# Optimization experiments

Measured on AMD Instinct MI355X. Metric: run time of the kernel, lower is better.

Reference implementation:

```python
import jax, jax.numpy as jnp
import numpy as np

B, S, H = 8, 2048, 2048

def setup_inputs() -> dict:
    key = jax.random.key(0)
    ks = jax.random.split(key, 7)
    return {
        "time_decay": jax.random.normal(ks[0], (H,), dtype=jnp.float32),
        "key": jax.random.normal(ks[1], (B, S, H), dtype=jnp.float32),
        "time_first": jax.random.normal(ks[2], (H,), dtype=jnp.float32),
        "value": jax.random.normal(ks[3], (B, S, H), dtype=jnp.float32),
        "max_state": jax.random.normal(ks[4], (B, H), dtype=jnp.float32),
        "num_state": jax.random.normal(ks[5], (B, H), dtype=jnp.float32),
        "den_state": jax.random.uniform(ks[6], (B, H), dtype=jnp.float32),
    }

def _wkv(time_decay, k, time_first, v, max_state, num_state, den_state):
    f32 = jnp.float32
    td = -jnp.exp(time_decay.astype(f32))          # [H]
    tf = time_first.astype(f32)                    # [H]
    k = k.astype(f32)
    v = v.astype(f32)

    def step(carry, kv_t):
        m, num, den = carry                        # each [B,H]
        kt, vt = kv_t                              # each [B,H]
        # output branch: include time_first bonus
        mo = jnp.maximum(m, kt + tf)
        e1o = jnp.exp(m - mo)
        e2o = jnp.exp(kt + tf - mo)
        out = (e1o * num + e2o * vt) / (e1o * den + e2o)
        # state branch: apply decay
        ms = jnp.maximum(m + td, kt)
        e1s = jnp.exp(m + td - ms)
        e2s = jnp.exp(kt - ms)
        return (ms, e1s * num + e2s * vt, e1s * den + e2s), out

    carry0 = (max_state.astype(f32), num_state.astype(f32), den_state.astype(f32))
    # scan over time: move seq axis to front -> [S,B,H]
    (m, num, den), outs = jax.lax.scan(
        step, carry0, (jnp.swapaxes(k, 0, 1), jnp.swapaxes(v, 0, 1)))
    output = jnp.swapaxes(outs, 0, 1)              # [B,S,H]
    return output, m, num, den

def reference(time_decay, key, time_first, value, max_state, num_state, den_state):
    return _wkv(time_decay, key, time_first, value, max_state, num_state, den_state)
```

## Files before the change

kernel.cpp:

```cpp
#include <hip/hip_runtime.h>


#define TILE 128
#define NW   16
#define SUB  (TILE / NW)

#define BARR  asm volatile("s_waitcnt lgkmcnt(0)\n\ts_barrier" ::: "memory")

__device__ __forceinline__ float ex2(float x)  { return __builtin_amdgcn_exp2f(x); }
__device__ __forceinline__ float rcpf(float x) { return __builtin_amdgcn_rcpf(x); }

__global__ __launch_bounds__(1024)
void wkv_fwd(const float* __restrict__ td_in, const float* __restrict__ kin,
             const float* __restrict__ tf_in, const float* __restrict__ vin,
             const float* __restrict__ m0, const float* __restrict__ n0,
             const float* __restrict__ d0,
             float* __restrict__ out, float* __restrict__ m_out,
             float* __restrict__ n_out, float* __restrict__ dn_out,
             int B, int S, int H)
{
    __shared__ float smry[2][NW][3][64];
    __shared__ float cry[2][3][64];

    const int tid  = threadIdx.x;
    const int lane = tid & 63;
    const int w    = tid >> 6;

    const int bpb = H >> 6;
    const int b   = blockIdx.x / bpb;
    const int hb  = (blockIdx.x - b * bpb) << 6;
    const int h   = hb + lane;
    const int g   = b * H + h;

    constexpr float Cc = 1.4426950408889634f;
    constexpr float IC = 0.6931471805599453f;

    const float tds  = -ex2(td_in[h] * Cc) * Cc;
    const float tfs  = tf_in[h] * Cc;
    const float dseg = tds * (float)SUB;

    if (w == 0) {
        cry[0][0][lane] = m0[g] * Cc;
        cry[0][1][lane] = n0[g];
        cry[0][2][lane] = d0[g];
    }

    const size_t base = (size_t)b * (size_t)S * (size_t)H + (size_t)hb;
    const float* gk = kin + base;
    const float* gv = vin + base;
    float*       go = out + base;

    const int ntiles = S / TILE;

    float fM = 0.f, fN = 0.f, fD = 0.f;

    float ka[SUB], va[SUB], kb[SUB], vb[SUB];

    {
        const size_t t0 = (size_t)w * SUB;
        #pragma unroll
        for (int j = 0; j < SUB; ++j) {
            ka[j] = gk[(t0 + j) * (size_t)H + lane];
            va[j] = gv[(t0 + j) * (size_t)H + lane];
        }
    }

    auto body = [&](int it, float (&ck)[SUB], float (&cv)[SUB],
                    float (&nk)[SUB], float (&nv)[SUB])
                __attribute__((always_inline)) -> void {
        if (it + 1 < ntiles) {
            const size_t t1 = (size_t)(it + 1) * TILE + (size_t)w * SUB;
            #pragma unroll
            for (int j = 0; j < SUB; ++j) {
                nk[j] = gk[(t1 + j) * (size_t)H + lane];
                nv[j] = gv[(t1 + j) * (size_t)H + lane];
            }
        }

        const int p = it & 1;

        float kt[SUB], vt[SUB];
        float plm[SUB - 1], pln[SUB - 1], pld[SUB - 1];
        float lm = -1e30f, ln = 0.f, ld = 0.f;
        #pragma unroll
        for (int j = 0; j < SUB; ++j) {
            kt[j] = ck[j] * Cc;
            vt[j] = cv[j];
            const float mpd = lm + tds;
            const float d   = mpd - kt[j];
            const float e   = ex2(-fabsf(d));
            const bool  c   = d >= 0.f;
            const float e1  = c ? 1.f : e;
            const float e2  = c ? e : 1.f;
            ln  = e1 * ln  + e2 * vt[j];
            ld  = e1 * ld  + e2;
            lm  = fmaxf(mpd, kt[j]);
            if (j < SUB - 1) { plm[j] = lm; pln[j] = ln; pld[j] = ld; }
        }
        smry[p][w][0][lane] = lm;
        smry[p][w][1][lane] = ln;
        smry[p][w][2][lane] = ld;
        BARR;

        float M = cry[p][0][lane];
        float N = cry[p][1][lane];
        float D = cry[p][2][lane];
        #pragma unroll
        for (int j = 0; j < NW - 1; ++j) {
            const float sm = smry[p][j][0][lane];
            const float sn = smry[p][j][1][lane];
            const float sd = smry[p][j][2][lane];
            if (j < w) {
                const float Md = M + dseg;
                const float d  = Md - sm;
                const float e  = ex2(-fabsf(d));
                const bool  c  = d >= 0.f;
                const float a  = c ? 1.f : e;
                const float bb = c ? e : 1.f;
                N = a * N + bb * sn;
                D = a * D + bb * sd;
                M = fmaxf(Md, sm);
            }
        }

        if (w == NW - 1) {
            const float Md = M + dseg;
            const float d  = Md - lm;
            const float e  = ex2(-fabsf(d));
            const bool  c  = d >= 0.f;
            const float a  = c ? 1.f : e;
            const float bb = c ? e : 1.f;
            fN = a * N + bb * ln;
            fD = a * D + bb * ld;
            fM = fmaxf(Md, lm);
            cry[p ^ 1][0][lane] = fM;
            cry[p ^ 1][1][lane] = fN;
            cry[p ^ 1][2][lane] = fD;
        }

        float* po = go + ((size_t)it * TILE + (size_t)w * SUB) * (size_t)H;
        {
            const float ktf = kt[0] + tfs;
            const float dd  = M - ktf;
            const float eo  = ex2(-fabsf(dd));
            const bool  co  = dd >= 0.f;
            const float e1o = co ? 1.f : eo;
            const float e2o = co ? eo : 1.f;
            po[lane] = (e1o * N + e2o * vt[0]) * rcpf(fmaf(e1o, D, e2o));
        }
        float Md = M;
        #pragma unroll
        for (int j = 1; j < SUB; ++j) {
            Md += tds;
            const float sm = plm[j - 1];
            const float dl = Md - sm;
            const float e  = ex2(-fabsf(dl));
            const bool  c  = dl >= 0.f;
            const float a  = c ? 1.f : e;
            const float bb = c ? e : 1.f;
            const float Nc = a * N + bb * pln[j - 1];
            const float Dc = a * D + bb * pld[j - 1];
            const float Mc = fmaxf(Md, sm);
            const float ktf = kt[j] + tfs;
            const float dd  = Mc - ktf;
            const float eo  = ex2(-fabsf(dd));
            const bool  co  = dd >= 0.f;
            const float e1o = co ? 1.f : eo;
            const float e2o = co ? eo : 1.f;
            po[(size_t)j * H + lane] =
                (e1o * Nc + e2o * vt[j]) * rcpf(fmaf(e1o, Dc, e2o));
        }
    };

    int it = 0;
    for (; it + 1 < ntiles; it += 2) {
        body(it,     ka, va, kb, vb);
        body(it + 1, kb, vb, ka, va);
    }
    if (it < ntiles) body(it, ka, va, kb, vb);

    if (w == NW - 1) {
        m_out[g]  = fM * IC;
        n_out[g]  = fN;
        dn_out[g] = fD;
    }
}

__global__ __launch_bounds__(64)
void wkv_fwd_serial(const float* __restrict__ td_in, const float* __restrict__ kin,
                    const float* __restrict__ tf_in, const float* __restrict__ vin,
                    const float* __restrict__ m0, const float* __restrict__ n0,
                    const float* __restrict__ d0,
                    float* __restrict__ out, float* __restrict__ m_out,
                    float* __restrict__ n_out, float* __restrict__ dn_out,
                    int B, int S, int H)
{
    const int g = blockIdx.x * 64 + threadIdx.x;
    if (g >= B * H) return;
    const int b = g / H;
    const int h = g - b * H;
    constexpr float Cc = 1.4426950408889634f, IC = 0.6931471805599453f;
    const float tds = -ex2(td_in[h] * Cc) * Cc;
    const float tfs = tf_in[h] * Cc;
    float M = m0[g] * Cc, N = n0[g], D = d0[g];
    const size_t base = (size_t)b * S * H + h;
    for (int t = 0; t < S; ++t) {
        const float kt  = kin[base + (size_t)t * H] * Cc;
        const float vt  = vin[base + (size_t)t * H];
        const float ktf = kt + tfs;
        const float mo  = fmaxf(M, ktf);
        const float e1o = ex2(M - mo), e2o = ex2(ktf - mo);
        out[base + (size_t)t * H] = (e1o * N + e2o * vt) * rcpf(e1o * D + e2o);
        const float mpd = M + tds;
        const float ms  = fmaxf(mpd, kt);
        const float e1s = ex2(mpd - ms), e2s = ex2(kt - ms);
        N = e1s * N + e2s * vt;
        D = e1s * D + e2s;
        M = ms;
    }
    m_out[g] = M * IC; n_out[g] = N; dn_out[g] = D;
}

extern "C" void kernel_launch(void* const* d_in, const int* in_sizes, int n_in,
                              void* d_out, int out_size, void* d_ws, size_t ws_size,
                              hipStream_t stream)
{
    const float* time_decay = (const float*)d_in[0];
    const float* key        = (const float*)d_in[1];
    const float* time_first = (const float*)d_in[2];
    const float* value      = (const float*)d_in[3];
    const float* max_state  = (const float*)d_in[4];
    const float* num_state  = (const float*)d_in[5];
    const float* den_state  = (const float*)d_in[6];

    const int H  = in_sizes[0];
    const int BH = in_sizes[4];
    const int B  = BH / H;
    const int S  = in_sizes[1] / BH;

    float* out    = (float*)d_out;
    float* m_out  = out + (size_t)B * (size_t)S * (size_t)H;
    float* n_out  = m_out + BH;
    float* dn_out = n_out + BH;

    if ((H % 64 == 0) && (S % TILE == 0)) {
        const int grid = BH / 64;
        wkv_fwd<<<grid, 1024, 0, stream>>>(time_decay, key, time_first, value,
                                           max_state, num_state, den_state,
                                           out, m_out, n_out, dn_out, B, S, H);
    } else {
        const int grid = (BH + 63) / 64;
        wkv_fwd_serial<<<grid, 64, 0, stream>>>(time_decay, key, time_first, value,
                                                max_state, num_state, den_state,
                                                out, m_out, n_out, dn_out, B, S, H);
    }
}
```

Before: 337.0 us.

## Split each wave across two time segments per 32-channel group with shuffle merge

Each block now covers 32 channels instead of 64. The two half-waves each scan a separate 8-step segment of a 256-step tile, and their summaries are merged with a cross-lane shuffle before the block-level scan. The per-step prefix states are no longer stored. Outputs are instead produced by re-running the recurrence from the merged segment prefix. The grid doubles, which raises parallelism and occupancy, at the cost of half-wave 32-float global accesses and an extra merge step.

Result: slower. 496.4 us (+47.3%).

```diff
diff --git a/kernel.cpp b/kernel.cpp
--- a/kernel.cpp
+++ b/kernel.cpp
@@ -1,16 +1,31 @@
 #include <hip/hip_runtime.h>
 
 
-#define TILE 128
-#define NW   16
-#define SUB  (TILE / NW)
+#define TILE   256
+#define NW     16
+#define WSTEPS 16
+#define SUBL   8
 
 #define BARR  asm volatile("s_waitcnt lgkmcnt(0)\n\ts_barrier" ::: "memory")
 
 __device__ __forceinline__ float ex2(float x)  { return __builtin_amdgcn_exp2f(x); }
 __device__ __forceinline__ float rcpf(float x) { return __builtin_amdgcn_rcpf(x); }
 
-__global__ __launch_bounds__(1024)
+__device__ __forceinline__ void merge(float& M, float& N, float& D,
+                                      float dlen, float sm, float sn, float sd)
+{
+    const float Md = M + dlen;
+    const float d  = Md - sm;
+    const float e  = ex2(-fabsf(d));
+    const bool  c  = d >= 0.f;
+    const float a  = c ? 1.f : e;
+    const float bb = c ? e : 1.f;
+    N = a * N + bb * sn;
+    D = a * D + bb * sd;
+    M = fmaxf(Md, sm);
+}
+
+__global__ __launch_bounds__(1024, 8)
 void wkv_fwd(const float* __restrict__ td_in, const float* __restrict__ kin,
              const float* __restrict__ tf_in, const float* __restrict__ vin,
              const float* __restrict__ m0, const float* __restrict__ n0,
@@ -19,30 +34,33 @@
              float* __restrict__ n_out, float* __restrict__ dn_out,
              int B, int S, int H)
 {
-    __shared__ float smry[2][NW][3][64];
-    __shared__ float cry[2][3][64];
+    __shared__ float smry[2][NW][3][32];
+    __shared__ float cry[2][3][32];
 
     const int tid  = threadIdx.x;
     const int lane = tid & 63;
     const int w    = tid >> 6;
-
-    const int bpb = H >> 6;
+    const int c    = lane & 31;
+    const int s    = lane >> 5;
+
+    const int bpb = H >> 5;
     const int b   = blockIdx.x / bpb;
-    const int hb  = (blockIdx.x - b * bpb) << 6;
-    const int h   = hb + lane;
+    const int hb  = (blockIdx.x - b * bpb) << 5;
+    const int h   = hb + c;
     const int g   = b * H + h;
 
     constexpr float Cc = 1.4426950408889634f;
     constexpr float IC = 0.6931471805599453f;
 
-    const float tds  = -ex2(td_in[h] * Cc) * Cc;
-    const float tfs  = tf_in[h] * Cc;
-    const float dseg = tds * (float)SUB;
-
-    if (w == 0) {
-        cry[0][0][lane] = m0[g] * Cc;
-        cry[0][1][lane] = n0[g];
-        cry[0][2][lane] = d0[g];
+    const float tds    = -ex2(td_in[h] * Cc) * Cc;
+    const float tfs    = tf_in[h] * Cc;
+    const float dseg8  = tds * (float)SUBL;
+    const float dseg16 = tds * (float)WSTEPS;
+
+    if (w == 0 && s == 0) {
+        cry[0][0][c] = m0[g] * Cc;
+        cry[0][1][c] = n0[g];
+        cry[0][2][c] = d0[g];
     }
 
     const size_t base = (size_t)b * (size_t)S * (size_t)H + (size_t)hb;
@@ -50,125 +68,111 @@
     const float* gv = vin + base;
     float*       go = out + base;
 
+    const int row0   = w * WSTEPS + s * SUBL;
     const int ntiles = S / TILE;
 
     float fM = 0.f, fN = 0.f, fD = 0.f;
 
-    float ka[SUB], va[SUB], kb[SUB], vb[SUB];
-
-    {
-        const size_t t0 = (size_t)w * SUB;
-        #pragma unroll
-        for (int j = 0; j < SUB; ++j) {
-            ka[j] = gk[(t0 + j) * (size_t)H + lane];
-            va[j] = gv[(t0 + j) * (size_t)H + lane];
-        }
-    }
-
-    auto body = [&](int it, float (&ck)[SUB], float (&cv)[SUB],
-                    float (&nk)[SUB], float (&nv)[SUB])
+    float ka[SUBL], va[SUBL], kb[SUBL], vb[SUBL];
+
+    #pragma unroll
+    for (int j = 0; j < SUBL; ++j) {
+        ka[j] = gk[(size_t)(row0 + j) * (size_t)H + c];
+        va[j] = gv[(size_t)(row0 + j) * (size_t)H + c];
+    }
+
+    auto body = [&](int it, float (&ck)[SUBL], float (&cv)[SUBL],
+                    float (&nk)[SUBL], float (&nv)[SUBL])
                 __attribute__((always_inline)) -> void {
         if (it + 1 < ntiles) {
-            const size_t t1 = (size_t)(it + 1) * TILE + (size_t)w * SUB;
+            const size_t r1 = (size_t)(it + 1) * TILE + row0;
             #pragma unroll
-            for (int j = 0; j < SUB; ++j) {
-                nk[j] = gk[(t1 + j) * (size_t)H + lane];
-                nv[j] = gv[(t1 + j) * (size_t)H + lane];
+            for (int j = 0; j < SUBL; ++j) {
+                nk[j] = gk[(r1 + j) * (size_t)H + c];
+                nv[j] = gv[(r1 + j) * (size_t)H + c];
             }
         }
 
         const int p = it & 1;
 
-        float kt[SUB], vt[SUB];
-        float plm[SUB - 1], pln[SUB - 1], pld[SUB - 1];
         float lm = -1e30f, ln = 0.f, ld = 0.f;
         #pragma unroll
-        for (int j = 0; j < SUB; ++j) {
-            kt[j] = ck[j] * Cc;
-            vt[j] = cv[j];
+        for (int j = 0; j < SUBL; ++j) {
+            const float kt = ck[j] * Cc;
+            ck[j] = kt;
+            const float vt  = cv[j];
             const float mpd = lm + tds;
-            const float d   = mpd - kt[j];
+            const float d   = mpd - kt;
             const float e   = ex2(-fabsf(d));
-            const bool  c   = d >= 0.f;
-            const float e1  = c ? 1.f : e;
-            const float e2  = c ? e : 1.f;
-            ln  = e1 * ln  + e2 * vt[j];
-            ld  = e1 * ld  + e2;
-            lm  = fmaxf(mpd, kt[j]);
-            if (j < SUB - 1) { plm[j] = lm; pln[j] = ln; pld[j] = ld; }
-        }
-        smry[p][w][0][lane] = lm;
-        smry[p][w][1][lane] = ln;
-        smry[p][w][2][lane] = ld;
+            const bool  cc  = d >= 0.f;
+            const float e1  = cc ? 1.f : e;
+            const float e2  = cc ? e : 1.f;
+            ln = e1 * ln + e2 * vt;
+            ld = e1 * ld + e2;
+            lm = fmaxf(mpd, kt);
+        }
+
+        const float om = __shfl_xor(lm, 32);
+        const float on = __shfl_xor(ln, 32);
+        const float od = __shfl_xor(ld, 32);
+
+        float wm = s ? om : lm, wn = s ? on : ln, wd = s ? od : ld;
+        {
+            const float sm2 = s ? lm : om;
+            const float sn2 = s ? ln : on;
+            const float sd2 = s ? ld : od;
+            merge(wm, wn, wd, dseg8, sm2, sn2, sd2);
+        }
+        if (s == 0) {
+            smry[p][w][0][c] = wm;
+            smry[p][w][1][c] = wn;
+            smry[p][w][2][c] = wd;
+        }
         BARR;
 
-        float M = cry[p][0][lane];
-        float N = cry[p][1][lane];
-        float D = cry[p][2][lane];
+        float M = cry[p][0][c];
+        float N = cry[p][1][c];
+        float D = cry[p][2][c];
         #pragma unroll
         for (int j = 0; j < NW - 1; ++j) {
-            const float sm = smry[p][j][0][lane];
-            const float sn = smry[p][j][1][lane];
-            const float sd = smry[p][j][2][lane];
-            if (j < w) {
-                const float Md = M + dseg;
-                const float d  = Md - sm;
-                const float e  = ex2(-fabsf(d));
-                const bool  c  = d >= 0.f;
-                const float a  = c ? 1.f : e;
-                const float bb = c ? e : 1.f;
-                N = a * N + bb * sn;
-                D = a * D + bb * sd;
-                M = fmaxf(Md, sm);
-            }
-        }
-
-        if (w == NW - 1) {
-            const float Md = M + dseg;
-            const float d  = Md - lm;
-            const float e  = ex2(-fabsf(d));
-            const bool  c  = d >= 0.f;
-            const float a  = c ? 1.f : e;
-            const float bb = c ? e : 1.f;
-            fN = a * N + bb * ln;
-            fD = a * D + bb * ld;
-            fM = fmaxf(Md, lm);
-            cry[p ^ 1][0][lane] = fM;
-            cry[p ^ 1][1][lane] = fN;
-            cry[p ^ 1][2][lane] = fD;
-        }
-
-        float* po = go + ((size_t)it * TILE + (size_t)w * SUB) * (size_t)H;
-        {
-            const float ktf = kt[0] + tfs;
+            const float sm = smry[p][j][0][c];
+            const float sn = smry[p][j][1][c];
+            const float sd = smry[p][j][2][c];
+            if (j < w) merge(M, N, D, dseg16, sm, sn, sd);
+        }
+
+        if (w == NW - 1 && s == 0) {
+            fM = M; fN = N; fD = D;
+            merge(fM, fN, fD, dseg16, wm, wn, wd);
+            cry[p ^ 1][0][c] = fM;
+            cry[p ^ 1][1][c] = fN;
+            cry[p ^ 1][2][c] = fD;
+        }
+
+        if (s == 1) merge(M, N, D, dseg8, om, on, od);
+
+        float* po = go + ((size_t)it * TILE + row0) * (size_t)H;
+        #pragma unroll
+        for (int j = 0; j < SUBL; ++j) {
+            const float kt  = ck[j];
+            const float vt  = cv[j];
+            const float ktf = kt + tfs;
             const float dd  = M - ktf;
             const float eo  = ex2(-fabsf(dd));
             const bool  co  = dd >= 0.f;
             const float e1o = co ? 1.f : eo;
             const float e2o = co ? eo : 1.f;
-            po[lane] = (e1o * N + e2o * vt[0]) * rcpf(fmaf(e1o, D, e2o));
-        }
-        float Md = M;
-        #pragma unroll
-        for (int j = 1; j < SUB; ++j) {
-            Md += tds;
-            const float sm = plm[j - 1];
-            const float dl = Md - sm;
-            const float e  = ex2(-fabsf(dl));
-            const bool  c  = dl >= 0.f;
-            const float a  = c ? 1.f : e;
-            const float bb = c ? e : 1.f;
-            const float Nc = a * N + bb * pln[j - 1];
-            const float Dc = a * D + bb * pld[j - 1];
-            const float Mc = fmaxf(Md, sm);
-            const float ktf = kt[j] + tfs;
-            const float dd  = Mc - ktf;
-            const float eo  = ex2(-fabsf(dd));
-            const bool  co  = dd >= 0.f;
-            const float e1o = co ? 1.f : eo;
-            const float e2o = co ? eo : 1.f;
-            po[(size_t)j * H + lane] =
-                (e1o * Nc + e2o * vt[j]) * rcpf(fmaf(e1o, Dc, e2o));
+            po[(size_t)j * H + c] =
+                (e1o * N + e2o * vt) * rcpf(fmaf(e1o, D, e2o));
+            const float mpd = M + tds;
+            const float ds_ = mpd - kt;
+            const float es  = ex2(-fabsf(ds_));
+            const bool  cs  = ds_ >= 0.f;
+            const float e1s = cs ? 1.f : es;
+            const float e2s = cs ? es : 1.f;
+            N = e1s * N + e2s * vt;
+            D = e1s * D + e2s;
+            M = fmaxf(mpd, kt);
         }
     };
 
@@ -179,7 +183,7 @@
     }
     if (it < ntiles) body(it, ka, va, kb, vb);
 
-    if (w == NW - 1) {
+    if (w == NW - 1 && s == 0) {
         m_out[g]  = fM * IC;
         n_out[g]  = fN;
         dn_out[g] = fD;
@@ -243,8 +247,8 @@
     float* n_out  = m_out + BH;
     float* dn_out = n_out + BH;
 
-    if ((H % 64 == 0) && (S % TILE == 0)) {
-        const int grid = BH / 64;
+    if ((H % 32 == 0) && (S % TILE == 0)) {
+        const int grid = BH / 32;
         wkv_fwd<<<grid, 1024, 0, stream>>>(time_decay, key, time_first, value,
                                            max_state, num_state, den_state,
                                            out, m_out, n_out, dn_out, B, S, H);
```

## Deepen k/v prefetch to two tiles ahead, remap blocks across XCDs, nontemporal stores

Applied to the files above, without the earlier changes.

The k/v register prefetch goes from double to triple buffering, so loads for tile it+2 are issued while tile it is computed. This hides more global-memory latency at the cost of more registers. Block IDs are remapped so consecutive logical blocks spread across the 8 XCDs, output stores become nontemporal to avoid polluting cache, and launch bounds now request a minimum occupancy. The higher register pressure combined with the occupancy hint may cause spills.

Result: slower. 527.5 us (+56.6%).

```diff
diff --git a/kernel.cpp b/kernel.cpp
--- a/kernel.cpp
+++ b/kernel.cpp
@@ -10,7 +10,7 @@
 __device__ __forceinline__ float ex2(float x)  { return __builtin_amdgcn_exp2f(x); }
 __device__ __forceinline__ float rcpf(float x) { return __builtin_amdgcn_rcpf(x); }
 
-__global__ __launch_bounds__(1024)
+__global__ __launch_bounds__(1024, 4)
 void wkv_fwd(const float* __restrict__ td_in, const float* __restrict__ kin,
              const float* __restrict__ tf_in, const float* __restrict__ vin,
              const float* __restrict__ m0, const float* __restrict__ n0,
@@ -26,9 +26,16 @@
     const int lane = tid & 63;
     const int w    = tid >> 6;
 
+    const int nwg = gridDim.x;
+    int bid = blockIdx.x;
+    if ((nwg & 7) == 0) {
+        const int cpx = nwg >> 3;
+        bid = (blockIdx.x & 7) * cpx + (blockIdx.x >> 3);
+    }
+
     const int bpb = H >> 6;
-    const int b   = blockIdx.x / bpb;
-    const int hb  = (blockIdx.x - b * bpb) << 6;
+    const int b   = bid / bpb;
+    const int hb  = (bid - b * bpb) << 6;
     const int h   = hb + lane;
     const int g   = b * H + h;
 
@@ -54,7 +61,7 @@
 
     float fM = 0.f, fN = 0.f, fD = 0.f;
 
-    float ka[SUB], va[SUB], kb[SUB], vb[SUB];
+    float ka[SUB], va[SUB], kb[SUB], vb[SUB], kc[SUB], vc[SUB];
 
     {
         const size_t t0 = (size_t)w * SUB;
@@ -63,17 +70,25 @@
             ka[j] = gk[(t0 + j) * (size_t)H + lane];
             va[j] = gv[(t0 + j) * (size_t)H + lane];
         }
-    }
-
-    auto body = [&](int it, float (&ck)[SUB], float (&cv)[SUB],
-                    float (&nk)[SUB], float (&nv)[SUB])
-                __attribute__((always_inline)) -> void {
-        if (it + 1 < ntiles) {
-            const size_t t1 = (size_t)(it + 1) * TILE + (size_t)w * SUB;
+        if (ntiles > 1) {
+            const size_t t1 = (size_t)TILE + (size_t)w * SUB;
             #pragma unroll
             for (int j = 0; j < SUB; ++j) {
-                nk[j] = gk[(t1 + j) * (size_t)H + lane];
-                nv[j] = gv[(t1 + j) * (size_t)H + lane];
+                kb[j] = gk[(t1 + j) * (size_t)H + lane];
+                vb[j] = gv[(t1 + j) * (size_t)H + lane];
+            }
+        }
+    }
+
+    auto body = [&](int it, float (&ck)[SUB], float (&cv)[SUB],
+                    float (&fk)[SUB], float (&fv)[SUB])
+                __attribute__((always_inline)) -> void {
+        if (it + 2 < ntiles) {
+            const size_t t2 = (size_t)(it + 2) * TILE + (size_t)w * SUB;
+            #pragma unroll
+            for (int j = 0; j < SUB; ++j) {
+                fk[j] = gk[(t2 + j) * (size_t)H + lane];
+                fv[j] = gv[(t2 + j) * (size_t)H + lane];
             }
         }
 
@@ -146,7 +161,8 @@
             const bool  co  = dd >= 0.f;
             const float e1o = co ? 1.f : eo;
             const float e2o = co ? eo : 1.f;
-            po[lane] = (e1o * N + e2o * vt[0]) * rcpf(fmaf(e1o, D, e2o));
+            __builtin_nontemporal_store(
+                (e1o * N + e2o * vt[0]) * rcpf(fmaf(e1o, D, e2o)), po + lane);
         }
         float Md = M;
         #pragma unroll
@@ -167,17 +183,20 @@
             const bool  co  = dd >= 0.f;
             const float e1o = co ? 1.f : eo;
             const float e2o = co ? eo : 1.f;
-            po[(size_t)j * H + lane] =
-                (e1o * Nc + e2o * vt[j]) * rcpf(fmaf(e1o, Dc, e2o));
+            __builtin_nontemporal_store(
+                (e1o * Nc + e2o * vt[j]) * rcpf(fmaf(e1o, Dc, e2o)),
+                po + (size_t)j * H + lane);
         }
     };
 
     int it = 0;
-    for (; it + 1 < ntiles; it += 2) {
-        body(it,     ka, va, kb, vb);
+    for (; it + 2 < ntiles; it += 3) {
+        body(it,     ka, va, kc, vc);
         body(it + 1, kb, vb, ka, va);
-    }
-    if (it < ntiles) body(it, ka, va, kb, vb);
+        body(it + 2, kc, vc, kb, vb);
+    }
+    if (it < ntiles) { body(it, ka, va, kc, vc); ++it; }
+    if (it < ntiles) { body(it, kb, vb, ka, va); }
 
     if (w == NW - 1) {
         m_out[g]  = fM * IC;
```
